# Optimization experiments

Hardware: AMD Instinct MI355X
Metric: run time of the kernel (lower is better)

Reference implementation:

```python
import jax, jax.numpy as jnp
import numpy as np

B, S, N_NODES, D_IN = 8, 24, 400, 3
D_MODEL = 32
G1_HEADS, G1_DIM = 4, 16
G2_HEADS, G2_DIM = 1, 32
T_KEY = 32


def _ln(x, g, b, eps=1e-6):
    m = jnp.mean(x, -1, keepdims=True)
    v = jnp.var(x, -1, keepdims=True)
    return g * (x - m) / jnp.sqrt(v + eps) + b


def _gat(x, adj, wq, bq, wk, bk, wv, bv, heads, dim):
    # x: [B*, N, F]; adjacency-masked multi-head attention (GraphAttention)
    Bx, N, _ = x.shape
    q = (x @ wq + bq).reshape(Bx, N, heads, dim)
    k = (x @ wk + bk).reshape(Bx, N, heads, dim)
    v = (x @ wv + bv).reshape(Bx, N, heads, dim)
    s = jnp.einsum('bihd,bjhd->bhij', q, k) / jnp.sqrt(jnp.float32(dim))
    s = jnp.where((adj == 0)[None, None], jnp.float32(-1e9), s)
    w = jax.nn.softmax(s, axis=-1)
    o = jnp.einsum('bhij,bjhd->bihd', w, v)
    return o.reshape(Bx, N, heads * dim)


def _mha(x, wq, bq, wk, bk, wv, bv, wo, bo):
    # keras MultiHeadAttention(num_heads=2, key_dim=32), self-attention, output dim = 32
    q = jnp.einsum('bsd,dhk->bshk', x, wq) + bq
    k = jnp.einsum('bsd,dhk->bshk', x, wk) + bk
    v = jnp.einsum('bsd,dhk->bshk', x, wv) + bv
    a = jax.nn.softmax(jnp.einsum('bqhk,bshk->bhqs', q, k) / jnp.sqrt(jnp.float32(T_KEY)), axis=-1)
    o = jnp.einsum('bhqs,bshk->bqhk', a, v)
    return jnp.einsum('bqhk,hko->bqo', o, wo) + bo


def setup_inputs() -> dict:
    ks = jax.random.split(jax.random.key(0), 20)

    def w(k, shape, scale=0.05):
        return (jax.random.normal(k, shape) * scale).astype(jnp.float32)

    z = lambda *s: jnp.zeros(s, jnp.float32)
    one = lambda *s: jnp.ones(s, jnp.float32)

    d = {}
    d['inputs'] = jax.random.normal(ks[0], (B, S, N_NODES, D_IN), dtype=jnp.float32)
    adj = (jax.random.uniform(ks[1], (N_NODES, N_NODES)) < 0.05).astype(jnp.float32)
    adj = jnp.minimum(adj + jnp.eye(N_NODES, dtype=jnp.float32), 1.0)
    d['adj'] = adj / (jnp.sum(adj, axis=1, keepdims=True) + 1e-6)  # row-normalized

    d['g1_wq'] = w(ks[2], (D_IN, G1_HEADS * G1_DIM)); d['g1_bq'] = z(G1_HEADS * G1_DIM)
    d['g1_wk'] = w(ks[3], (D_IN, G1_HEADS * G1_DIM)); d['g1_bk'] = z(G1_HEADS * G1_DIM)
    d['g1_wv'] = w(ks[4], (D_IN, G1_HEADS * G1_DIM)); d['g1_bv'] = z(G1_HEADS * G1_DIM)
    d['g2_wq'] = w(ks[5], (G1_HEADS * G1_DIM, G2_DIM)); d['g2_bq'] = z(G2_DIM)
    d['g2_wk'] = w(ks[6], (G1_HEADS * G1_DIM, G2_DIM)); d['g2_bk'] = z(G2_DIM)
    d['g2_wv'] = w(ks[7], (G1_HEADS * G1_DIM, G2_DIM)); d['g2_bv'] = z(G2_DIM)
    d['sp_g'] = one(D_MODEL); d['sp_b'] = z(D_MODEL)
    d['t_wq'] = w(ks[8], (D_MODEL, 2, T_KEY)); d['t_bq'] = z(2, T_KEY)
    d['t_wk'] = w(ks[9], (D_MODEL, 2, T_KEY)); d['t_bk'] = z(2, T_KEY)
    d['t_wv'] = w(ks[10], (D_MODEL, 2, T_KEY)); d['t_bv'] = z(2, T_KEY)
    d['t_wo'] = w(ks[11], (2, T_KEY, D_MODEL)); d['t_bo'] = z(D_MODEL)
    d['ff_w1'] = w(ks[12], (D_MODEL, 64)); d['ff_b1'] = z(64)
    d['ff_w2'] = w(ks[13], (64, D_MODEL)); d['ff_b2'] = z(D_MODEL)
    d['ln1_g'] = one(D_MODEL); d['ln1_b'] = z(D_MODEL)
    d['ln2_g'] = one(D_MODEL); d['ln2_b'] = z(D_MODEL)
    d['fin_g'] = one(D_MODEL); d['fin_b'] = z(D_MODEL)
    d['fd_w'] = w(ks[14], (D_MODEL, 1), scale=0.01); d['fd_b'] = z(1)
    return d


def reference(inputs, adj, g1_wq, g1_bq, g1_wk, g1_bk, g1_wv, g1_bv,
              g2_wq, g2_bq, g2_wk, g2_bk, g2_wv, g2_bv, sp_g, sp_b,
              t_wq, t_bq, t_wk, t_bk, t_wv, t_bv, t_wo, t_bo,
              ff_w1, ff_b1, ff_w2, ff_b2, ln1_g, ln1_b, ln2_g, ln2_b,
              fin_g, fin_b, fd_w, fd_b):
    Bx, Sx, N, _ = inputs.shape
    x = inputs.reshape(Bx * Sx, N, D_IN)

    # SpatialProcessor: GAT1 -> relu -> GAT2 -> residual layernorm
    h = jax.nn.relu(_gat(x, adj, g1_wq, g1_bq, g1_wk, g1_bk, g1_wv, g1_bv, G1_HEADS, G1_DIM))
    h = _gat(h, adj, g2_wq, g2_bq, g2_wk, g2_bk, g2_wv, g2_bv, G2_HEADS, G2_DIM)
    res = jnp.pad(x, ((0, 0), (0, 0), (0, D_MODEL - D_IN)))  # zero-pad 3 -> 32 for residual
    sp = _ln(h + res, sp_g, sp_b)
    sp4 = sp.reshape(Bx, Sx, N, D_MODEL)  # [B, S, N, 32]

    # TemporalTransformer over sequence per node
    t_in = jnp.transpose(sp4, (0, 2, 1, 3)).reshape(Bx * N, Sx, D_MODEL)
    a = _mha(t_in, t_wq, t_bq, t_wk, t_bk, t_wv, t_bv, t_wo, t_bo)
    x1 = _ln(t_in + a, ln1_g, ln1_b)
    f = jax.nn.gelu(x1 @ ff_w1 + ff_b1, approximate=False) @ ff_w2 + ff_b2
    t_out = _ln(x1 + f, ln2_g, ln2_b).reshape(Bx, N, Sx, D_MODEL)

    # fuse: mean over seq (spatial) + mean over seq (temporal), layernorm, final dense
    fused = _ln(jnp.mean(sp4, axis=1) + jnp.mean(t_out, axis=2), fin_g, fin_b)
    return (fused @ fd_w + fd_b)[..., 0]  # [B, N]
```

## Files before the change

### kernel.cpp

```cpp
#include <hip/hip_runtime.h>
#include <hip/hip_bf16.h>

#define NN 400
#define KMAX 64

struct WTab {
  const void* p[34];
  int off[35];
};

__device__ __forceinline__ float bflo(unsigned u) {
  union { unsigned i; float f; } x; x.i = u << 16; return x.f;
}
__device__ __forceinline__ float bfhi(unsigned u) {
  union { unsigned i; float f; } x; x.i = u & 0xffff0000u; return x.f;
}
__device__ __forceinline__ unsigned short f2bf(float f) {
  __hip_bfloat16 b = __float2bfloat16(f);
  return *reinterpret_cast<unsigned short*>(&b);
}
__device__ __forceinline__ unsigned packbf(float a, float b) {
  return (unsigned)f2bf(a) | ((unsigned)f2bf(b) << 16);
}
__device__ __forceinline__ bool detect_bf16(const unsigned short* probe) {
  int lane = threadIdx.x & 63;
  unsigned short u = probe[lane * 2];
  int e = (u >> 7) & 0xFF;
  bool plaus = (u == 0) || (e >= 112 && e <= 132);
  return __popcll(__ballot(plaus)) >= 48;
}
__device__ __forceinline__ float rsum32(float v) {
  v += __shfl_xor(v, 1); v += __shfl_xor(v, 2); v += __shfl_xor(v, 4);
  v += __shfl_xor(v, 8); v += __shfl_xor(v, 16); return v;
}

__global__ void convert_w_k(WTab wt, const unsigned short* __restrict__ probe,
                            float* __restrict__ dst) {
  bool isbf = detect_bf16(probe);
  int total = wt.off[34];
  for (int i = blockIdx.x * blockDim.x + threadIdx.x; i < total;
       i += gridDim.x * blockDim.x) {
    int lo = 0, hi = 33;
    while (lo < hi) {
      int mid = (lo + hi + 1) >> 1;
      if (i >= wt.off[mid]) lo = mid; else hi = mid - 1;
    }
    int rel = i - wt.off[lo];
    float v;
    if (isbf) v = __bfloat162float(((const __hip_bfloat16*)wt.p[lo])[rel]);
    else      v = ((const float*)wt.p[lo])[rel];
    dst[i] = v;
  }
}

__global__ void build_csr_k(const void* __restrict__ adj,
                            const unsigned short* __restrict__ probe,
                            int* __restrict__ colp, int* __restrict__ degp) {
  bool isbf = detect_bf16(probe);
  int row = blockIdx.x, lane = threadIdx.x;
  int base = 0;
  for (int j0 = 0; j0 < NN; j0 += 64) {
    int j = j0 + lane;
    bool nz;
    if (isbf) nz = (j < NN) && ((const unsigned short*)adj)[row * NN + j] != 0;
    else      nz = (j < NN) && ((const float*)adj)[row * NN + j] != 0.0f;
    unsigned long long m = __ballot(nz);
    int offl = __popcll(m & ((1ull << lane) - 1ull));
    if (nz) {
      int pidx = base + offl;
      if (pidx < KMAX) colp[row * KMAX + pidx] = j;
    }
    base += __popcll(m);
  }
  if (lane == 0) degp[row] = base < KMAX ? base : KMAX;
}

__global__ __launch_bounds__(256) void gat1_k(
    const void* __restrict__ xraw, const unsigned short* __restrict__ probe,
    const float* __restrict__ g1, const int* __restrict__ colp,
    const int* __restrict__ degp, unsigned short* __restrict__ h1b) {
  __shared__ float xsf[NN * 4];
  __shared__ float yhf[4 * NN * 4];
  __shared__ float w1s[768];
  __shared__ float cf[64];
  const int tid = threadIdx.x;
  const int g = blockIdx.x;
  bool isbf = detect_bf16(probe);

  for (int e = tid; e < 768; e += 256) w1s[e] = g1[e];
  for (int e = tid; e < NN; e += 256) xsf[e * 4 + 3] = 0.f;
  for (int e = tid; e < NN * 3; e += 256) {
    int j = e / 3, a = e - j * 3;
    float v;
    if (isbf) v = __bfloat162float(((const __hip_bfloat16*)xraw)[g * NN * 3 + e]);
    else      v = ((const float*)xraw)[g * NN * 3 + e];
    xsf[j * 4 + a] = v;
  }
  __syncthreads();

  if (tid < 64) {
    int h = tid >> 4, t = tid & 15, co = h * 16;
    float acc = 0.f;
    if (t < 9) {
      int a = t / 3, b = t - (t / 3) * 3;
      for (int c = 0; c < 16; ++c) acc += w1s[a * 64 + co + c] * w1s[256 + b * 64 + co + c];
    } else if (t < 12) {
      int a = t - 9;
      for (int c = 0; c < 16; ++c) acc += w1s[a * 64 + co + c] * w1s[448 + co + c];
    } else if (t < 15) {
      int b = t - 12;
      for (int c = 0; c < 16; ++c) acc += w1s[256 + b * 64 + co + c] * w1s[192 + co + c];
    } else {
      for (int c = 0; c < 16; ++c) acc += w1s[192 + co + c] * w1s[448 + co + c];
    }
    cf[h * 16 + t] = acc;
  }
  __syncthreads();

  for (int e = tid; e < NN * 4; e += 256) {
    int j = e >> 2, h = e & 3;
    const float* bse = cf + h * 16;
    float x0 = xsf[j * 4], x1 = xsf[j * 4 + 1], x2 = xsf[j * 4 + 2];
    float* y = yhf + (h * NN + j) * 4;
    y[0] = bse[0] * x0 + bse[1] * x1 + bse[2] * x2;
    y[1] = bse[3] * x0 + bse[4] * x1 + bse[5] * x2;
    y[2] = bse[6] * x0 + bse[7] * x1 + bse[8] * x2;
    y[3] = bse[12] * x0 + bse[13] * x1 + bse[14] * x2 + bse[15];
  }
  __syncthreads();

  const float4* xs4 = (const float4*)xsf;
  const float4* yh4 = (const float4*)yhf;
  for (int i = tid; i < NN; i += 256) {
    float4 xi = xs4[i];
    float ch[4];
    #pragma unroll
    for (int h = 0; h < 4; ++h)
      ch[h] = cf[h * 16 + 9] * xi.x + cf[h * 16 + 10] * xi.y + cf[h * 16 + 11] * xi.z;
    float l[4] = {0.f, 0.f, 0.f, 0.f};
    float ax[4], ay[4], az[4];
    #pragma unroll
    for (int h = 0; h < 4; ++h) { ax[h] = 0.f; ay[h] = 0.f; az[h] = 0.f; }
    int dg = degp[i];
    const int* cols = colp + i * KMAX;
    for (int e = 0; e < dg; ++e) {
      int j = cols[e];
      float4 xj = xs4[j];
      #pragma unroll
      for (int h = 0; h < 4; ++h) {
        float4 y = yh4[h * NN + j];
        float s = (xi.x * y.x + xi.y * y.y + xi.z * y.z + y.w + ch[h]) * 0.25f;
        float p = __expf(s);
        l[h] += p;
        ax[h] += p * xj.x; ay[h] += p * xj.y; az[h] += p * xj.z;
      }
    }
    unsigned* hr = (unsigned*)(h1b + ((size_t)g * NN + i) * 64);
    #pragma unroll
    for (int h = 0; h < 4; ++h) {
      float inv = 1.f / l[h];
      float b0 = ax[h] * inv, b1 = ay[h] * inv, b2 = az[h] * inv;
      int co = h * 16;
      #pragma unroll
      for (int c = 0; c < 16; c += 2) {
        float o0 = fmaxf(b0 * w1s[512 + co + c] + b1 * w1s[576 + co + c] +
                         b2 * w1s[640 + co + c] + w1s[704 + co + c], 0.f);
        float o1 = fmaxf(b0 * w1s[513 + co + c] + b1 * w1s[577 + co + c] +
                         b2 * w1s[641 + co + c] + w1s[705 + co + c], 0.f);
        hr[(co + c) >> 1] = packbf(o0, o1);
      }
    }
  }
}

__global__ __launch_bounds__(256) void gat2_proj_k(
    const unsigned short* __restrict__ h1b, const float* __restrict__ g2,
    unsigned short* __restrict__ q2b, unsigned short* __restrict__ k2g,
    unsigned short* __restrict__ v2g) {
  __shared__ float ht[64 * 68];
  __shared__ float wqs[2048], wks[2048], wvs[2048];
  __shared__ float bqs[32], bks[32], bvs[32];
  const int tid = threadIdx.x, t = blockIdx.x;
  for (int e = tid; e < 2048; e += 256) {
    unsigned u = ((const unsigned*)h1b)[t * 2048 + e];
    int ln = e >> 5, d0 = (e & 31) * 2;
    ht[d0 * 68 + ln] = bflo(u);
    ht[(d0 + 1) * 68 + ln] = bfhi(u);
  }
  for (int e = tid; e < 2048; e += 256) {
    wqs[e] = g2[e]; wks[e] = g2[2080 + e]; wvs[e] = g2[4160 + e];
  }
  if (tid < 32) { bqs[tid] = g2[2048 + tid]; bks[tid] = g2[4128 + tid]; bvs[tid] = g2[6208 + tid]; }
  __syncthreads();
  const int c = tid & 31, ng = tid >> 5;
  float qa[8], ka[8], va[8];
  #pragma unroll
  for (int k = 0; k < 8; ++k) { qa[k] = bqs[c]; ka[k] = bks[c]; va[k] = bvs[c]; }
  for (int d = 0; d < 64; ++d) {
    float wq = wqs[d * 32 + c], wk = wks[d * 32 + c], wv = wvs[d * 32 + c];
    const float4* hp = (const float4*)(ht + d * 68 + ng * 8);
    float4 h0 = hp[0], h1v = hp[1];
    float hv[8] = {h0.x, h0.y, h0.z, h0.w, h1v.x, h1v.y, h1v.z, h1v.w};
    #pragma unroll
    for (int k = 0; k < 8; ++k) {
      qa[k] += hv[k] * wq; ka[k] += hv[k] * wk; va[k] += hv[k] * wv;
    }
  }
  #pragma unroll
  for (int k = 0; k < 8; ++k) {
    int gn = t * 64 + ng * 8 + k;
    q2b[gn * 32 + c] = f2bf(qa[k]);
    k2g[gn * 32 + c] = f2bf(ka[k]);
    v2g[gn * 32 + c] = f2bf(va[k]);
  }
}

__global__ __launch_bounds__(256) void gat2_attn_k(
    const void* __restrict__ xraw, const unsigned short* __restrict__ probe,
    const unsigned short* __restrict__ q2b, const unsigned short* __restrict__ k2g,
    const unsigned short* __restrict__ v2g, const float* __restrict__ spw,
    const int* __restrict__ colp, const int* __restrict__ degp,
    float* __restrict__ spo) {
  __shared__ unsigned short k2s[NN * 40];
  __shared__ unsigned short v2s[NN * 40];
  __shared__ float gw[64];
  const int tid = threadIdx.x;
  const int g = blockIdx.x;
  bool isbf = detect_bf16(probe);
  if (tid < 64) gw[tid] = spw[tid];
  for (int e = tid; e < 6400; e += 256) {
    unsigned uk = ((const unsigned*)k2g)[g * 6400 + e];
    unsigned uv = ((const unsigned*)v2g)[g * 6400 + e];
    int n = e >> 4, c = e & 15;
    ((unsigned*)k2s)[n * 20 + c] = uk;
    ((unsigned*)v2s)[n * 20 + c] = uv;
  }
  __syncthreads();
  const int b = g / 24, st = g % 24;
  for (int i = tid; i < NN; i += 256) {
    const uint4* qp = (const uint4*)(q2b + ((size_t)g * NN + i) * 32);
    uint4 qw[4] = {qp[0], qp[1], qp[2], qp[3]};
    float q[32], o[32];
    #pragma unroll
    for (int t = 0; t < 4; ++t) {
      unsigned uu[4] = {qw[t].x, qw[t].y, qw[t].z, qw[t].w};
      #pragma unroll
      for (int m = 0; m < 4; ++m) {
        q[t * 8 + 2 * m] = bflo(uu[m]); q[t * 8 + 2 * m + 1] = bfhi(uu[m]);
      }
    }
    #pragma unroll
    for (int c = 0; c < 32; ++c) o[c] = 0.f;
    int dg = degp[i];
    const int* cols = colp + i * KMAX;
    float l = 0.f;
    for (int e = 0; e < dg; ++e) {
      int j = cols[e];
      const uint4* kr = (const uint4*)(k2s + j * 40);
      const uint4* vr = (const uint4*)(v2s + j * 40);
      float s = 0.f;
      #pragma unroll
      for (int t = 0; t < 4; ++t) {
        uint4 kk = kr[t];
        unsigned uu[4] = {kk.x, kk.y, kk.z, kk.w};
        #pragma unroll
        for (int m = 0; m < 4; ++m)
          s += q[t * 8 + 2 * m] * bflo(uu[m]) + q[t * 8 + 2 * m + 1] * bfhi(uu[m]);
      }
      float p = __expf(s * 0.17677669529663688f);
      l += p;
      #pragma unroll
      for (int t = 0; t < 4; ++t) {
        uint4 vv = vr[t];
        unsigned uu[4] = {vv.x, vv.y, vv.z, vv.w};
        #pragma unroll
        for (int m = 0; m < 4; ++m) {
          o[t * 8 + 2 * m]     += p * bflo(uu[m]);
          o[t * 8 + 2 * m + 1] += p * bfhi(uu[m]);
        }
      }
    }
    float inv = 1.f / l;
    float xr[3];
    #pragma unroll
    for (int a = 0; a < 3; ++a) {
      if (isbf) xr[a] = __bfloat162float(((const __hip_bfloat16*)xraw)[((size_t)g * NN + i) * 3 + a]);
      else      xr[a] = ((const float*)xraw)[((size_t)g * NN + i) * 3 + a];
    }
    float row[32];
    #pragma unroll
    for (int c = 0; c < 32; ++c) row[c] = o[c] * inv;
    row[0] += xr[0]; row[1] += xr[1]; row[2] += xr[2];
    float mean = 0.f;
    #pragma unroll
    for (int c = 0; c < 32; ++c) mean += row[c];
    mean *= (1.f / 32.f);
    float var = 0.f;
    #pragma unroll
    for (int c = 0; c < 32; ++c) { float dd = row[c] - mean; var += dd * dd; }
    var *= (1.f / 32.f);
    float rinv = 1.f / sqrtf(var + 1e-6f);
    float4* so4 = (float4*)(spo + (((size_t)b * NN + i) * 24 + st) * 32);
    #pragma unroll
    for (int k = 0; k < 8; ++k) {
      float4 v;
      v.x = gw[4 * k]     * (row[4 * k]     - mean) * rinv + gw[32 + 4 * k];
      v.y = gw[4 * k + 1] * (row[4 * k + 1] - mean) * rinv + gw[33 + 4 * k];
      v.z = gw[4 * k + 2] * (row[4 * k + 2] - mean) * rinv + gw[34 + 4 * k];
      v.w = gw[4 * k + 3] * (row[4 * k + 3] - mean) * rinv + gw[35 + 4 * k];
      so4[k] = v;
    }
  }
}

__global__ __launch_bounds__(128) void temporal_k(
    const float* __restrict__ sp, const float* __restrict__ tw,
    const unsigned short* __restrict__ probe, void* __restrict__ outp) {
  __shared__ float sm[7728];
  float* t_s = sm;
  float* q_s = sm + 768;
  float* k_s = sm + 2400;
  float* v_s = sm + 4032;
  float* aw  = sm + 5664;
  float* x1s = sm + 6864;
  float* att = q_s;
  float* f1s = k_s;
  const int tid = threadIdx.x;
  bool isbf = detect_bf16(probe);

  const float* twq = tw;            const float* tbq = tw + 2048;
  const float* twk = tw + 2112;     const float* tbk = tw + 4160;
  const float* twv = tw + 4224;     const float* tbv = tw + 6272;
  const float* two = tw + 6336;     const float* tbo = tw + 8384;
  const float* fw1 = tw + 8416;     const float* fb1 = tw + 10464;
  const float* fw2 = tw + 10528;    const float* fb2 = tw + 12576;
  const float* l1g = tw + 12608;    const float* l1b = tw + 12640;
  const float* l2g = tw + 12672;    const float* l2b = tw + 12704;
  const float* fng = tw + 12736;    const float* fnb = tw + 12768;
  const float* fdw = tw + 12800;    const float* fdb = tw + 12832;

  const float4* base4 = (const float4*)(sp + (size_t)blockIdx.x * 768);
  for (int e = tid; e < 192; e += 128) ((float4*)t_s)[e] = base4[e];
  __syncthreads();

  {
    const int hk = tid & 63, sh = tid >> 6;
    float wq[32], wk[32], wv[32];
    #pragma unroll
    for (int c = 0; c < 32; ++c) {
      wq[c] = twq[c * 64 + hk]; wk[c] = twk[c * 64 + hk]; wv[c] = twv[c * 64 + hk];
    }
    float bq = tbq[hk], bk = tbk[hk], bv = tbv[hk];
    for (int s = sh * 12; s < sh * 12 + 12; ++s) {
      const float4* tr4 = (const float4*)(t_s + s * 32);
      float tt[32];
      #pragma unroll
      for (int k = 0; k < 8; ++k) { float4 t4 = tr4[k];
        tt[4*k] = t4.x; tt[4*k+1] = t4.y; tt[4*k+2] = t4.z; tt[4*k+3] = t4.w; }
      float qa = bq, ka = bk, va = bv;
      #pragma unroll
      for (int c = 0; c < 32; ++c) {
        qa += tt[c] * wq[c]; ka += tt[c] * wk[c]; va += tt[c] * wv[c];
      }
      q_s[s * 68 + hk] = qa; k_s[s * 68 + hk] = ka; v_s[s * 68 + hk] = va;
    }
  }
  __syncthreads();

  {
    const int h = tid >> 6, l = tid & 63;
    if (l < 48) {
      const int qs = l >> 1, half = l & 1;
      const float4* qr4 = (const float4*)(q_s + qs * 68 + h * 32);
      float qv[32];
      #pragma unroll
      for (int k = 0; k < 8; ++k) { float4 t4 = qr4[k];
        qv[4*k] = t4.x; qv[4*k+1] = t4.y; qv[4*k+2] = t4.z; qv[4*k+3] = t4.w; }
      float sc[12], lsum = 0.f;
      #pragma unroll
      for (int k = 0; k < 12; ++k) {
        const float4* kr4 = (const float4*)(k_s + (half * 12 + k) * 68 + h * 32);
        float s = 0.f;
        #pragma unroll
        for (int m = 0; m < 8; ++m) {
          float4 kk = kr4[m];
          s += qv[4*m] * kk.x + qv[4*m+1] * kk.y + qv[4*m+2] * kk.z + qv[4*m+3] * kk.w;
        }
        sc[k] = __expf(s * 0.17677669529663688f);
        lsum += sc[k];
      }
      lsum += __shfl_xor(lsum, 1);
      float inv = 1.f / lsum;
      float* ar = aw + (h * 24 + qs) * 25 + half * 12;
      #pragma unroll
      for (int k = 0; k < 12; ++k) ar[k] = sc[k] * inv;
    }
  }
  __syncthreads();

  {
    const int g = tid >> 4, hkq = tid & 15, h = hkq >> 3;
    float4 acc[3];
    #pragma unroll
    for (int m = 0; m < 3; ++m) acc[m] = make_float4(0.f, 0.f, 0.f, 0.f);
    const float4* vs4 = (const float4*)v_s;
    for (int ss = 0; ss < 24; ++ss) {
      float4 v4 = vs4[ss * 17 + hkq];
      #pragma unroll
      for (int m = 0; m < 3; ++m) {
        float a = aw[(h * 24 + g + 8 * m) * 25 + ss];
        acc[m].x += a * v4.x; acc[m].y += a * v4.y;
        acc[m].z += a * v4.z; acc[m].w += a * v4.w;
      }
    }
    #pragma unroll
    for (int m = 0; m < 3; ++m) ((float4*)att)[(g + 8 * m) * 17 + hkq] = acc[m];
  }
  __syncthreads();

  {
    const int c = tid & 31, half = (tid >> 5) & 1, w = tid >> 6;
    float wcol[64];
    #pragma unroll
    for (int hk = 0; hk < 64; ++hk) wcol[hk] = two[hk * 32 + c];
    float bo = tbo[c], g1c = l1g[c], b1c = l1b[c];
    #pragma unroll
    for (int k = 0; k < 6; ++k) {
      int s = (w * 2 + half) + 4 * k;
      const float4* ar4 = (const float4*)(att + s * 68);
      float acc = bo;
      #pragma unroll
      for (int jj = 0; jj < 16; ++jj) {
        float4 av = ar4[jj];
        acc += av.x * wcol[4*jj] + av.y * wcol[4*jj+1] +
               av.z * wcol[4*jj+2] + av.w * wcol[4*jj+3];
      }
      float val = t_s[s * 32 + c] + acc;
      float mean = rsum32(val) * (1.f / 32.f);
      float dv = val - mean;
      float var = rsum32(dv * dv) * (1.f / 32.f);
      float ri = 1.f / sqrtf(var + 1e-6f);
      x1s[s * 36 + c] = g1c * dv * ri + b1c;
    }
  }
  __syncthreads();

  {
    const int j = tid & 63, sh = tid >> 6;
    float w[32];
    #pragma unroll
    for (int c = 0; c < 32; ++c) w[c] = fw1[c * 64 + j];
    float bias = fb1[j];
    for (int s = sh * 12; s < sh * 12 + 12; ++s) {
      const float4* xr4 = (const float4*)(x1s + s * 36);
      float acc = bias;
      #pragma unroll
      for (int m = 0; m < 8; ++m) {
        float4 xv = xr4[m];
        acc += xv.x * w[4*m] + xv.y * w[4*m+1] + xv.z * w[4*m+2] + xv.w * w[4*m+3];
      }
      f1s[s * 68 + j] = 0.5f * acc * (1.f + erff(acc * 0.70710678118654752f));
    }
  }
  __syncthreads();

  {
    const int c = tid & 31, half = (tid >> 5) & 1, w = tid >> 6;
    float wcol[64];
    #pragma unroll
    for (int j = 0; j < 64; ++j) wcol[j] = fw2[j * 32 + c];
    float b2 = fb2[c], g2c = l2g[c], b2c = l2b[c];
    #pragma unroll
    for (int k = 0; k < 6; ++k) {
      int s = (w * 2 + half) + 4 * k;
      const float4* fr4 = (const float4*)(f1s + s * 68);
      float acc = b2;
      #pragma unroll
      for (int jj = 0; jj < 16; ++jj) {
        float4 fv = fr4[jj];
        acc += fv.x * wcol[4*jj] + fv.y * wcol[4*jj+1] +
               fv.z * wcol[4*jj+2] + fv.w * wcol[4*jj+3];
      }
      float val = x1s[s * 36 + c] + acc;
      float mean = rsum32(val) * (1.f / 32.f);
      float dv = val - mean;
      float var = rsum32(dv * dv) * (1.f / 32.f);
      float ri = 1.f / sqrtf(var + 1e-6f);
      x1s[s * 36 + c] = g2c * dv * ri + b2c;
    }
  }
  __syncthreads();

  if (tid < 32) {
    const int c = tid;
    float ms = 0.f, mt = 0.f;
    #pragma unroll
    for (int s = 0; s < 24; ++s) { ms += t_s[s * 32 + c]; mt += x1s[s * 36 + c]; }
    float red = (ms + mt) * (1.f / 24.f);
    float mean = rsum32(red) * (1.f / 32.f);
    float dv = red - mean;
    float var = rsum32(dv * dv) * (1.f / 32.f);
    float ri = 1.f / sqrtf(var + 1e-6f);
    float y = (fng[c] * dv * ri + fnb[c]) * fdw[c];
    float tot = rsum32(y);
    if (c == 0) {
      float acc = tot + fdb[0];
      if (isbf) ((__hip_bfloat16*)outp)[blockIdx.x] = __float2bfloat16(acc);
      else      ((float*)outp)[blockIdx.x] = acc;
    }
  }
}

extern "C" void kernel_launch(void* const* d_in, const int* in_sizes, int n_in,
                              void* d_out, int out_size, void* d_ws, size_t ws_size,
                              hipStream_t stream) {
  static const int wsizes[34] = {
      192, 64, 192, 64, 192, 64,
      2048, 32, 2048, 32, 2048, 32,
      32, 32,
      2048, 64, 2048, 64, 2048, 64, 2048, 32,
      2048, 64, 2048, 32,
      32, 32, 32, 32, 32, 32,
      32, 1};
  WTab wt;
  int off = 0;
  for (int i = 0; i < 34; ++i) { wt.p[i] = d_in[i + 2]; wt.off[i] = off; off += wsizes[i]; }
  wt.off[34] = off;

  char* ws = (char*)d_ws;
  float* convw = (float*)ws;
  int*   colp  = (int*)(ws + 81920);
  int*   degp  = (int*)(ws + 184320);
  unsigned short* h1b = (unsigned short*)(ws + 196608);
  float*          spo = (float*)(ws + 196608);
  unsigned short* q2b = (unsigned short*)(ws + 10027008);
  unsigned short* k2g = (unsigned short*)(ws + 14942208);
  unsigned short* v2g = (unsigned short*)(ws + 19857408);

  const float* g1  = convw;
  const float* g2  = convw + 768;
  const float* spw = convw + 7008;
  const float* twp = convw + 7072;
  const unsigned short* probe = (const unsigned short*)d_in[0];

  hipLaunchKernelGGL(convert_w_k, dim3(40), dim3(256), 0, stream, wt, probe, convw);
  hipLaunchKernelGGL(build_csr_k, dim3(NN), dim3(64), 0, stream, d_in[1], probe,
                     colp, degp);
  hipLaunchKernelGGL(gat1_k, dim3(192), dim3(256), 0, stream, d_in[0], probe, g1,
                     (const int*)colp, (const int*)degp, h1b);
  hipLaunchKernelGGL(gat2_proj_k, dim3(1200), dim3(256), 0, stream,
                     (const unsigned short*)h1b, g2, q2b, k2g, v2g);
  hipLaunchKernelGGL(gat2_attn_k, dim3(192), dim3(256), 0, stream, d_in[0], probe,
                     (const unsigned short*)q2b, (const unsigned short*)k2g,
                     (const unsigned short*)v2g, spw, (const int*)colp,
                     (const int*)degp, spo);
  hipLaunchKernelGGL(temporal_k, dim3(3200), dim3(128), 0, stream,
                     (const float*)spo, twp, probe, d_out);
}
```

Before: 359.8 us.

## Merge prep kernels, split GAT rows across blocks, shrink temporal LDS with bf16

Merges weight conversion and CSR construction into one prep kernel, removing a launch. GAT1 and GAT2 attention now split the 400 nodes across two blocks in grid.y, so twice as many blocks fill the GPU, at the cost of each block restaging its full per-graph shared data. In the temporal kernel, Q/K/V and attention weights are stored in shared memory as bf16, cutting LDS per block to raise occupancy, but this adds rounding error. The output projection and FFN2 drop their register-held weight columns for direct global reads, and the layernorm becomes a serial per-row loop run by 24 threads.

After: 398.2 us. +10.7%, slower.

```diff
diff --git a/kernel.cpp b/kernel.cpp
--- a/kernel.cpp
+++ b/kernel.cpp
@@ -14,6 +14,9 @@
 }
 __device__ __forceinline__ float bfhi(unsigned u) {
   union { unsigned i; float f; } x; x.i = u & 0xffff0000u; return x.f;
+}
+__device__ __forceinline__ float bfu16(unsigned short u) {
+  union { unsigned i; float f; } x; x.i = ((unsigned)u) << 16; return x.f;
 }
 __device__ __forceinline__ unsigned short f2bf(float f) {
   __hip_bfloat16 b = __float2bfloat16(f);
@@ -34,45 +37,45 @@
   v += __shfl_xor(v, 8); v += __shfl_xor(v, 16); return v;
 }
 
-__global__ void convert_w_k(WTab wt, const unsigned short* __restrict__ probe,
-                            float* __restrict__ dst) {
+__global__ __launch_bounds__(256) void prep_k(
+    WTab wt, const void* __restrict__ adj,
+    const unsigned short* __restrict__ probe, float* __restrict__ dst,
+    int* __restrict__ colp, int* __restrict__ degp) {
   bool isbf = detect_bf16(probe);
-  int total = wt.off[34];
-  for (int i = blockIdx.x * blockDim.x + threadIdx.x; i < total;
-       i += gridDim.x * blockDim.x) {
-    int lo = 0, hi = 33;
-    while (lo < hi) {
-      int mid = (lo + hi + 1) >> 1;
-      if (i >= wt.off[mid]) lo = mid; else hi = mid - 1;
-    }
-    int rel = i - wt.off[lo];
-    float v;
-    if (isbf) v = __bfloat162float(((const __hip_bfloat16*)wt.p[lo])[rel]);
-    else      v = ((const float*)wt.p[lo])[rel];
-    dst[i] = v;
-  }
-}
-
-__global__ void build_csr_k(const void* __restrict__ adj,
-                            const unsigned short* __restrict__ probe,
-                            int* __restrict__ colp, int* __restrict__ degp) {
-  bool isbf = detect_bf16(probe);
-  int row = blockIdx.x, lane = threadIdx.x;
-  int base = 0;
-  for (int j0 = 0; j0 < NN; j0 += 64) {
-    int j = j0 + lane;
-    bool nz;
-    if (isbf) nz = (j < NN) && ((const unsigned short*)adj)[row * NN + j] != 0;
-    else      nz = (j < NN) && ((const float*)adj)[row * NN + j] != 0.0f;
-    unsigned long long m = __ballot(nz);
-    int offl = __popcll(m & ((1ull << lane) - 1ull));
-    if (nz) {
-      int pidx = base + offl;
-      if (pidx < KMAX) colp[row * KMAX + pidx] = j;
-    }
-    base += __popcll(m);
-  }
-  if (lane == 0) degp[row] = base < KMAX ? base : KMAX;
+  const int tid = threadIdx.x;
+  if (blockIdx.x < 40) {
+    int total = wt.off[34];
+    for (int i = blockIdx.x * 256 + tid; i < total; i += 40 * 256) {
+      int lo = 0, hi = 33;
+      while (lo < hi) {
+        int mid = (lo + hi + 1) >> 1;
+        if (i >= wt.off[mid]) lo = mid; else hi = mid - 1;
+      }
+      int rel = i - wt.off[lo];
+      float v;
+      if (isbf) v = __bfloat162float(((const __hip_bfloat16*)wt.p[lo])[rel]);
+      else      v = ((const float*)wt.p[lo])[rel];
+      dst[i] = v;
+    }
+  } else {
+    int row = (blockIdx.x - 40) * 4 + (tid >> 6);
+    int lane = tid & 63;
+    int base = 0;
+    for (int j0 = 0; j0 < NN; j0 += 64) {
+      int j = j0 + lane;
+      bool nz;
+      if (isbf) nz = (j < NN) && ((const unsigned short*)adj)[row * NN + j] != 0;
+      else      nz = (j < NN) && ((const float*)adj)[row * NN + j] != 0.0f;
+      unsigned long long m = __ballot(nz);
+      int offl = __popcll(m & ((1ull << lane) - 1ull));
+      if (nz) {
+        int pidx = base + offl;
+        if (pidx < KMAX) colp[row * KMAX + pidx] = j;
+      }
+      base += __popcll(m);
+    }
+    if (lane == 0) degp[row] = base < KMAX ? base : KMAX;
+  }
 }
 
 __global__ __launch_bounds__(256) void gat1_k(
@@ -131,7 +134,8 @@
 
   const float4* xs4 = (const float4*)xsf;
   const float4* yh4 = (const float4*)yhf;
-  for (int i = tid; i < NN; i += 256) {
+  const int i0 = blockIdx.y * 200;
+  for (int i = i0 + tid; i < i0 + 200; i += 256) {
     float4 xi = xs4[i];
     float ch[4];
     #pragma unroll
@@ -237,7 +241,8 @@
   }
   __syncthreads();
   const int b = g / 24, st = g % 24;
-  for (int i = tid; i < NN; i += 256) {
+  const int i0 = blockIdx.y * 200;
+  for (int i = i0 + tid; i < i0 + 200; i += 256) {
     const uint4* qp = (const uint4*)(q2b + ((size_t)g * NN + i) * 32);
     uint4 qw[4] = {qp[0], qp[1], qp[2], qp[3]};
     float q[32], o[32];
@@ -316,15 +321,13 @@
 __global__ __launch_bounds__(128) void temporal_k(
     const float* __restrict__ sp, const float* __restrict__ tw,
     const unsigned short* __restrict__ probe, void* __restrict__ outp) {
-  __shared__ float sm[7728];
-  float* t_s = sm;
-  float* q_s = sm + 768;
-  float* k_s = sm + 2400;
-  float* v_s = sm + 4032;
-  float* aw  = sm + 5664;
-  float* x1s = sm + 6864;
-  float* att = q_s;
-  float* f1s = k_s;
+  __shared__ float sm[4800];
+  unsigned short* smh = (unsigned short*)sm;
+  const unsigned* smu = (const unsigned*)sm;
+  float* att = sm;
+  float* f1s = sm + 1632;
+  float* x1s = sm + 3168;
+  float* t_s = sm + 4032;
   const int tid = threadIdx.x;
   bool isbf = detect_bf16(probe);
 
@@ -345,24 +348,21 @@
 
   {
     const int hk = tid & 63, sh = tid >> 6;
-    float wq[32], wk[32], wv[32];
-    #pragma unroll
-    for (int c = 0; c < 32; ++c) {
-      wq[c] = twq[c * 64 + hk]; wk[c] = twk[c * 64 + hk]; wv[c] = twv[c * 64 + hk];
-    }
-    float bq = tbq[hk], bk = tbk[hk], bv = tbv[hk];
-    for (int s = sh * 12; s < sh * 12 + 12; ++s) {
-      const float4* tr4 = (const float4*)(t_s + s * 32);
-      float tt[32];
-      #pragma unroll
-      for (int k = 0; k < 8; ++k) { float4 t4 = tr4[k];
-        tt[4*k] = t4.x; tt[4*k+1] = t4.y; tt[4*k+2] = t4.z; tt[4*k+3] = t4.w; }
-      float qa = bq, ka = bk, va = bv;
-      #pragma unroll
-      for (int c = 0; c < 32; ++c) {
-        qa += tt[c] * wq[c]; ka += tt[c] * wk[c]; va += tt[c] * wv[c];
-      }
-      q_s[s * 68 + hk] = qa; k_s[s * 68 + hk] = ka; v_s[s * 68 + hk] = va;
+    for (int a = 0; a < 3; ++a) {
+      const float* W  = (a == 0) ? twq : (a == 1) ? twk : twv;
+      const float* Bb = (a == 0) ? tbq : (a == 1) ? tbk : tbv;
+      const int ub = a * 816 * 2;
+      float w[32];
+      #pragma unroll
+      for (int c = 0; c < 32; ++c) w[c] = W[c * 64 + hk];
+      float bias = Bb[hk];
+      for (int s = sh * 12; s < sh * 12 + 12; ++s) {
+        const float* tr = t_s + s * 32;
+        float acc = bias;
+        #pragma unroll
+        for (int c = 0; c < 32; ++c) acc += tr[c] * w[c];
+        smh[ub + s * 68 + hk] = f2bf(acc);
+      }
     }
   }
   __syncthreads();
@@ -371,29 +371,32 @@
     const int h = tid >> 6, l = tid & 63;
     if (l < 48) {
       const int qs = l >> 1, half = l & 1;
-      const float4* qr4 = (const float4*)(q_s + qs * 68 + h * 32);
-      float qv[32];
-      #pragma unroll
-      for (int k = 0; k < 8; ++k) { float4 t4 = qr4[k];
-        qv[4*k] = t4.x; qv[4*k+1] = t4.y; qv[4*k+2] = t4.z; qv[4*k+3] = t4.w; }
+      const uint4* qr4 = (const uint4*)(smu + qs * 34 + h * 16);
+      uint4 qa = qr4[0], qb = qr4[1];
+      float qv[16];
+      {
+        unsigned uu[8] = {qa.x, qa.y, qa.z, qa.w, qb.x, qb.y, qb.z, qb.w};
+        #pragma unroll
+        for (int m = 0; m < 8; ++m) { qv[2*m] = bflo(uu[m]); qv[2*m+1] = bfhi(uu[m]); }
+      }
       float sc[12], lsum = 0.f;
       #pragma unroll
       for (int k = 0; k < 12; ++k) {
-        const float4* kr4 = (const float4*)(k_s + (half * 12 + k) * 68 + h * 32);
+        const uint4* kr4 = (const uint4*)(smu + 816 + (half * 12 + k) * 34 + h * 16);
+        uint4 ka = kr4[0], kb = kr4[1];
+        unsigned uu[8] = {ka.x, ka.y, ka.z, ka.w, kb.x, kb.y, kb.z, kb.w};
         float s = 0.f;
         #pragma unroll
-        for (int m = 0; m < 8; ++m) {
-          float4 kk = kr4[m];
-          s += qv[4*m] * kk.x + qv[4*m+1] * kk.y + qv[4*m+2] * kk.z + qv[4*m+3] * kk.w;
-        }
+        for (int m = 0; m < 8; ++m)
+          s += qv[2*m] * bflo(uu[m]) + qv[2*m+1] * bfhi(uu[m]);
         sc[k] = __expf(s * 0.17677669529663688f);
         lsum += sc[k];
       }
       lsum += __shfl_xor(lsum, 1);
       float inv = 1.f / lsum;
-      float* ar = aw + (h * 24 + qs) * 25 + half * 12;
-      #pragma unroll
-      for (int k = 0; k < 12; ++k) ar[k] = sc[k] * inv;
+      #pragma unroll
+      for (int k = 0; k < 12; ++k)
+        smh[4896 + (h * 24 + qs) * 25 + half * 12 + k] = f2bf(sc[k] * inv);
     }
   }
   __syncthreads();
@@ -403,45 +406,41 @@
     float4 acc[3];
     #pragma unroll
     for (int m = 0; m < 3; ++m) acc[m] = make_float4(0.f, 0.f, 0.f, 0.f);
-    const float4* vs4 = (const float4*)v_s;
     for (int ss = 0; ss < 24; ++ss) {
-      float4 v4 = vs4[ss * 17 + hkq];
+      uint2 vv = *(const uint2*)(smu + 1632 + ss * 34 + hkq * 2);
+      float v0 = bflo(vv.x), v1 = bfhi(vv.x), v2 = bflo(vv.y), v3 = bfhi(vv.y);
       #pragma unroll
       for (int m = 0; m < 3; ++m) {
-        float a = aw[(h * 24 + g + 8 * m) * 25 + ss];
-        acc[m].x += a * v4.x; acc[m].y += a * v4.y;
-        acc[m].z += a * v4.z; acc[m].w += a * v4.w;
-      }
-    }
-    #pragma unroll
-    for (int m = 0; m < 3; ++m) ((float4*)att)[(g + 8 * m) * 17 + hkq] = acc[m];
-  }
-  __syncthreads();
-
-  {
-    const int c = tid & 31, half = (tid >> 5) & 1, w = tid >> 6;
-    float wcol[64];
-    #pragma unroll
-    for (int hk = 0; hk < 64; ++hk) wcol[hk] = two[hk * 32 + c];
-    float bo = tbo[c], g1c = l1g[c], b1c = l1b[c];
-    #pragma unroll
-    for (int k = 0; k < 6; ++k) {
-      int s = (w * 2 + half) + 4 * k;
-      const float4* ar4 = (const float4*)(att + s * 68);
-      float acc = bo;
-      #pragma unroll
-      for (int jj = 0; jj < 16; ++jj) {
-        float4 av = ar4[jj];
-        acc += av.x * wcol[4*jj] + av.y * wcol[4*jj+1] +
-               av.z * wcol[4*jj+2] + av.w * wcol[4*jj+3];
-      }
-      float val = t_s[s * 32 + c] + acc;
-      float mean = rsum32(val) * (1.f / 32.f);
-      float dv = val - mean;
-      float var = rsum32(dv * dv) * (1.f / 32.f);
-      float ri = 1.f / sqrtf(var + 1e-6f);
-      x1s[s * 36 + c] = g1c * dv * ri + b1c;
-    }
+        float a = bfu16(smh[4896 + (h * 24 + g + 8 * m) * 25 + ss]);
+        acc[m].x += a * v0; acc[m].y += a * v1;
+        acc[m].z += a * v2; acc[m].w += a * v3;
+      }
+    }
+    #pragma unroll
+    for (int m = 0; m < 3; ++m)
+      *(float4*)(att + (g + 8 * m) * 68 + hkq * 4) = acc[m];
+  }
+  __syncthreads();
+
+  for (int e = tid; e < 768; e += 128) {
+    int s = e >> 5, c = e & 31;
+    const float* ar = att + s * 68;
+    float a = tbo[c];
+    #pragma unroll 8
+    for (int hk = 0; hk < 64; ++hk) a += ar[hk] * two[hk * 32 + c];
+    x1s[s * 36 + c] = t_s[s * 32 + c] + a;
+  }
+  __syncthreads();
+  if (tid < 24) {
+    float* r = x1s + tid * 36;
+    float mean = 0.f;
+    for (int c = 0; c < 32; ++c) mean += r[c];
+    mean *= (1.f / 32.f);
+    float var = 0.f;
+    for (int c = 0; c < 32; ++c) { float d = r[c] - mean; var += d * d; }
+    var *= (1.f / 32.f);
+    float ri = 1.f / sqrtf(var + 1e-6f);
+    for (int c = 0; c < 32; ++c) r[c] = l1g[c] * (r[c] - mean) * ri + l1b[c];
   }
   __syncthreads();
 
@@ -459,35 +458,30 @@
         float4 xv = xr4[m];
         acc += xv.x * w[4*m] + xv.y * w[4*m+1] + xv.z * w[4*m+2] + xv.w * w[4*m+3];
       }
-      f1s[s * 68 + j] = 0.5f * acc * (1.f + erff(acc * 0.70710678118654752f));
-    }
-  }
-  __syncthreads();
-
-  {
-    const int c = tid & 31, half = (tid >> 5) & 1, w = tid >> 6;
-    float wcol[64];
-    #pragma unroll
-    for (int j = 0; j < 64; ++j) wcol[j] = fw2[j * 32 + c];
-    float b2 = fb2[c], g2c = l2g[c], b2c = l2b[c];
-    #pragma unroll
-    for (int k = 0; k < 6; ++k) {
-      int s = (w * 2 + half) + 4 * k;
-      const float4* fr4 = (const float4*)(f1s + s * 68);
-      float acc = b2;
-      #pragma unroll
-      for (int jj = 0; jj < 16; ++jj) {
-        float4 fv = fr4[jj];
-        acc += fv.x * wcol[4*jj] + fv.y * wcol[4*jj+1] +
-               fv.z * wcol[4*jj+2] + fv.w * wcol[4*jj+3];
-      }
-      float val = x1s[s * 36 + c] + acc;
-      float mean = rsum32(val) * (1.f / 32.f);
-      float dv = val - mean;
-      float var = rsum32(dv * dv) * (1.f / 32.f);
-      float ri = 1.f / sqrtf(var + 1e-6f);
-      x1s[s * 36 + c] = g2c * dv * ri + b2c;
-    }
+      f1s[s * 64 + j] = 0.5f * acc * (1.f + erff(acc * 0.70710678118654752f));
+    }
+  }
+  __syncthreads();
+
+  for (int e = tid; e < 768; e += 128) {
+    int s = e >> 5, c = e & 31;
+    const float* fr = f1s + s * 64;
+    float a = fb2[c];
+    #pragma unroll 8
+    for (int j = 0; j < 64; ++j) a += fr[j] * fw2[j * 32 + c];
+    x1s[s * 36 + c] = x1s[s * 36 + c] + a;
+  }
+  __syncthreads();
+  if (tid < 24) {
+    float* r = x1s + tid * 36;
+    float mean = 0.f;
+    for (int c = 0; c < 32; ++c) mean += r[c];
+    mean *= (1.f / 32.f);
+    float var = 0.f;
+    for (int c = 0; c < 32; ++c) { float d = r[c] - mean; var += d * d; }
+    var *= (1.f / 32.f);
+    float ri = 1.f / sqrtf(var + 1e-6f);
+    for (int c = 0; c < 32; ++c) r[c] = l2g[c] * (r[c] - mean) * ri + l2b[c];
   }
   __syncthreads();
 
@@ -543,15 +537,14 @@
   const float* twp = convw + 7072;
   const unsigned short* probe = (const unsigned short*)d_in[0];
 
-  hipLaunchKernelGGL(convert_w_k, dim3(40), dim3(256), 0, stream, wt, probe, convw);
-  hipLaunchKernelGGL(build_csr_k, dim3(NN), dim3(64), 0, stream, d_in[1], probe,
-                     colp, degp);
-  hipLaunchKernelGGL(gat1_k, dim3(192), dim3(256), 0, stream, d_in[0], probe, g1,
-                     (const int*)colp, (const int*)degp, h1b);
+  hipLaunchKernelGGL(prep_k, dim3(140), dim3(256), 0, stream, wt, d_in[1], probe,
+                     convw, colp, degp);
+  hipLaunchKernelGGL(gat1_k, dim3(192, 2), dim3(256), 0, stream, d_in[0], probe,
+                     g1, (const int*)colp, (const int*)degp, h1b);
   hipLaunchKernelGGL(gat2_proj_k, dim3(1200), dim3(256), 0, stream,
                      (const unsigned short*)h1b, g2, q2b, k2g, v2g);
-  hipLaunchKernelGGL(gat2_attn_k, dim3(192), dim3(256), 0, stream, d_in[0], probe,
-                     (const unsigned short*)q2b, (const unsigned short*)k2g,
+  hipLaunchKernelGGL(gat2_attn_k, dim3(192, 2), dim3(256), 0, stream, d_in[0],
+                     probe, (const unsigned short*)q2b, (const unsigned short*)k2g,
                      (const unsigned short*)v2g, spw, (const int*)colp,
                      (const int*)degp, spo);
   hipLaunchKernelGGL(temporal_k, dim3(3200), dim3(128), 0, stream,
```
